# Kernel tuning notes

Hardware: AMD Instinct MI355X
Metric: run time of the kernel (lower is better)

Reference implementation:

```python
import jax, jax.numpy as jnp
import numpy as np

D_MODEL = 1024
D_K = 64
D_V = 64
N_HEADS = 16
LN_EPS = 1e-5


def setup_inputs() -> dict:
    key = jax.random.key(0)
    ks = jax.random.split(key, 9)
    B, S = 2, 2048
    scale = 0.02
    return {
        "input_Q": jax.random.normal(ks[0], (B, S, D_MODEL), dtype=jnp.float32),
        "input_K": jax.random.normal(ks[1], (B, S, D_MODEL), dtype=jnp.float32),
        "input_V": jax.random.normal(ks[2], (B, S, D_MODEL), dtype=jnp.float32),
        "W_Q": jax.random.normal(ks[3], (D_MODEL, N_HEADS * D_K), dtype=jnp.float32) * scale,
        "W_K": jax.random.normal(ks[4], (D_MODEL, N_HEADS * D_K), dtype=jnp.float32) * scale,
        "W_V": jax.random.normal(ks[5], (D_MODEL, N_HEADS * D_V), dtype=jnp.float32) * scale,
        "W_O": jax.random.normal(ks[6], (N_HEADS * D_V, D_MODEL), dtype=jnp.float32) * scale,
        "ln_gamma": jnp.ones((D_MODEL,), dtype=jnp.float32),
        "ln_beta": jnp.zeros((D_MODEL,), dtype=jnp.float32),
    }


def reference(input_Q, input_K, input_V, W_Q, W_K, W_V, W_O, ln_gamma, ln_beta):
    B, Lq, _ = input_Q.shape
    Lk = input_K.shape[1]
    # projections -> [B, H, L, d]
    Q = (input_Q @ W_Q).reshape(B, Lq, N_HEADS, D_K).transpose(0, 2, 1, 3)
    K = (input_K @ W_K).reshape(B, Lk, N_HEADS, D_K).transpose(0, 2, 1, 3)
    V = (input_V @ W_V).reshape(B, Lk, N_HEADS, D_V).transpose(0, 2, 1, 3)
    # scores: [B, H, Lq, Lk]
    scores = jnp.einsum("bhqd,bhkd->bhqk", Q, K) / jnp.sqrt(jnp.float32(D_K))
    # NOTE: source uses nn.Softmax(dim=1) -> softmax over the HEADS axis (faithful quirk)
    attn = jax.nn.softmax(scores, axis=1)
    context = jnp.einsum("bhqk,bhkv->bhqv", attn, V)
    context = context.transpose(0, 2, 1, 3).reshape(B, Lq, N_HEADS * D_V)
    output = context @ W_O
    # residual + LayerNorm over last dim
    x = output + input_Q
    mu = jnp.mean(x, axis=-1, keepdims=True)
    var = jnp.mean(jnp.square(x - mu), axis=-1, keepdims=True)
    return (x - mu) / jnp.sqrt(var + LN_EPS) * ln_gamma + ln_beta
```

## Files before the change

### kernel.cpp

```cpp
#include <hip/hip_runtime.h>
#include <cstdint>
#include <cstddef>

#define DM 1024
#define HEADS 16
#define DHEAD 64
#define SEQ 2048
#define BATCH 2

typedef __bf16 bf16x8 __attribute__((ext_vector_type(8)));
typedef float  f32x4  __attribute__((ext_vector_type(4)));
typedef unsigned short u16;
typedef unsigned int u32;
typedef u16 u16x8 __attribute__((ext_vector_type(8)));
typedef u16 u16x4 __attribute__((ext_vector_type(4)));

__device__ __forceinline__ float bf2f(u16 u){
    union { u32 i; float f; } v; v.i = ((u32)u) << 16; return v.f;
}
__device__ __forceinline__ u16 f2bf(float f){
    union { float f; u32 i; } v; v.f = f;
    u32 r = v.i + 0x7FFF + ((v.i >> 16) & 1);
    return (u16)(r >> 16);
}
__device__ __forceinline__ u16 f2bf_rhu(float f){
    union { float f; u32 i; } v; v.f = f;
    return (u16)((v.i + 0x8000u) >> 16);
}
__device__ __forceinline__ void gload16(const u16* g, u16* l){
    __builtin_amdgcn_global_load_lds(
        (const __attribute__((address_space(1))) u32*)g,
        (__attribute__((address_space(3))) u32*)l, 16, 0, 0);
}

__global__ void k_probe(const u16* __restrict__ q, int* __restrict__ hdr){
    if (threadIdx.x == 0 && blockIdx.x == 0){
        int cnt = 0;
        for (int i = 0; i < 256; i += 2){
            int e = (q[i] >> 7) & 0xFF;
            if (e >= 90 && e <= 141) cnt++;
        }
        hdr[0] = (cnt >= 64) ? 1 : 0;
        #pragma unroll
        for (int c = 1; c <= 8; c++) hdr[c] = 0;
    }
}

__global__ __launch_bounds__(256) void k_cvt3(const void* __restrict__ s0,
                                              const void* __restrict__ s1,
                                              const void* __restrict__ s2,
                                              u16* __restrict__ dstbase,
                                              const int* __restrict__ flag, int n){
    int z = blockIdx.y;
    const void* src = (z == 0) ? s0 : ((z == 1) ? s1 : s2);
    u16* dst = dstbase + (size_t)z * n;
    int i = (blockIdx.x * 256 + threadIdx.x) * 8;
    if (i >= n) return;
    if (*flag){
        *(u16x8*)&dst[i] = *(const u16x8*)((const u16*)src + i);
    } else {
        const float* s = (const float*)src + i;
        u16x8 o;
        #pragma unroll
        for (int j = 0; j < 8; j++) o[j] = f2bf(s[j]);
        *(u16x8*)&dst[i] = o;
    }
}

__global__ void k_tcvt4(const void* __restrict__ w0, const void* __restrict__ w1,
                        const void* __restrict__ w2, const void* __restrict__ w3,
                        u16* __restrict__ dstbase,
                        const int* __restrict__ flag, int R, int C){
    __shared__ u16 tile[32][33];
    int z = blockIdx.z;
    const void* src = (z == 0) ? w0 : ((z == 1) ? w1 : ((z == 2) ? w2 : w3));
    u16* dst = dstbase + (size_t)z * R * C;
    bool isbf = (*flag != 0);
    int c0 = blockIdx.x * 32, r0 = blockIdx.y * 32;
    int tx = threadIdx.x, ty = threadIdx.y;
    #pragma unroll
    for (int i = 0; i < 32; i += 8){
        size_t idx = (size_t)(r0 + ty + i) * C + c0 + tx;
        tile[ty + i][tx] = isbf ? ((const u16*)src)[idx] : f2bf(((const float*)src)[idx]);
    }
    __syncthreads();
    #pragma unroll
    for (int i = 0; i < 32; i += 8)
        dst[(size_t)(c0 + ty + i) * R + r0 + tx] = tile[tx][ty + i];
}

__global__ void k_transpose(const u16* __restrict__ src, u16* __restrict__ dst,
                            int R, int C){
    __shared__ u16 tile[32][33];
    size_t boff = (size_t)blockIdx.z * R * C;
    src += boff; dst += boff;
    int c0 = blockIdx.x * 32, r0 = blockIdx.y * 32;
    int tx = threadIdx.x, ty = threadIdx.y;
    #pragma unroll
    for (int i = 0; i < 32; i += 8)
        tile[ty + i][tx] = src[(size_t)(r0 + ty + i) * C + c0 + tx];
    __syncthreads();
    #pragma unroll
    for (int i = 0; i < 32; i += 8)
        dst[(size_t)(c0 + ty + i) * R + r0 + tx] = tile[tx][ty + i];
}

__global__ __launch_bounds__(256, 2) void k_gemm3z(const u16* __restrict__ A0,
                                                   const u16* __restrict__ Bt0,
                                                   u16* __restrict__ C0,
                                                   size_t strA, size_t strB, size_t strC,
                                                   int M, int N, int K){
    __shared__ u16 lsA[128 * 32];
    __shared__ u16 lsB[128 * 32];
    int z = blockIdx.z;
    const u16* A  = A0  + strA * z;
    const u16* Bt = Bt0 + strB * z;
    u16* C = C0 + strC * z;
    int m0 = blockIdx.y * 128, n0 = blockIdx.x * 128;
    int t = threadIdx.x, lane = t & 63, w = t >> 6;
    int l15 = lane & 15, quad = lane >> 4;
    int wm = (w & 1) * 64, wn = (w >> 1) * 64;
    int r0 = 32 * w + (lane >> 2);
    int r1 = r0 + 16;
    int c0s = (lane & 3) ^ (r0 & 3);
    int c1s = (lane & 3) ^ (r1 & 3);
    u16* dA0 = &lsA[(32 * w) * 32];
    u16* dA1 = &lsA[(32 * w + 16) * 32];
    u16* dB0 = &lsB[(32 * w) * 32];
    u16* dB1 = &lsB[(32 * w + 16) * 32];
    f32x4 acc[4][4] = {};
    for (int k0 = 0; k0 < K; k0 += 32){
        __syncthreads();
        gload16(&A [(size_t)(m0 + r0) * K + k0 + c0s * 8], dA0);
        gload16(&A [(size_t)(m0 + r1) * K + k0 + c1s * 8], dA1);
        gload16(&Bt[(size_t)(n0 + r0) * K + k0 + c0s * 8], dB0);
        gload16(&Bt[(size_t)(n0 + r1) * K + k0 + c1s * 8], dB1);
        __syncthreads();
        bf16x8 af[4], bfr[4];
        #pragma unroll
        for (int i = 0; i < 4; i++){
            int row = wm + i * 16 + l15;
            af[i] = *(const bf16x8*)&lsA[row * 32 + ((quad ^ (row & 3)) * 8)];
        }
        #pragma unroll
        for (int j = 0; j < 4; j++){
            int row = wn + j * 16 + l15;
            bfr[j] = *(const bf16x8*)&lsB[row * 32 + ((quad ^ (row & 3)) * 8)];
        }
        #pragma unroll
        for (int i = 0; i < 4; i++)
            #pragma unroll
            for (int j = 0; j < 4; j++)
                acc[i][j] = __builtin_amdgcn_mfma_f32_16x16x32_bf16(af[i], bfr[j], acc[i][j], 0, 0, 0);
    }
    #pragma unroll
    for (int i = 0; i < 4; i++)
        #pragma unroll
        for (int j = 0; j < 4; j++)
            #pragma unroll
            for (int r = 0; r < 4; r++){
                int m = m0 + wm + i * 16 + quad * 4 + r;
                int n = n0 + wn + j * 16 + l15;
                C[(size_t)m * N + n] = f2bf(acc[i][j][r]);
            }
}

__global__ __launch_bounds__(1024, 4) void k_attn5(const u16* __restrict__ Qp,
                                                   const u16* __restrict__ Kp,
                                                   const u16* __restrict__ Vt,
                                                   u16* __restrict__ c0,
                                                   u16* __restrict__ c1,
                                                   u16* __restrict__ c2,
                                                   u16* __restrict__ c3,
                                                   int* __restrict__ cnt,
                                                   int ncomboM1, int iters){
    __shared__ u16 ebuf[2][16][64][36];
    __shared__ int s_combo, s_slot;
    int t = threadIdx.x;
    if (t == 0){
        int xcc;
        asm volatile("s_getreg_b32 %0, hwreg(HW_REG_XCC_ID)" : "=s"(xcc));
        int start = xcc & ncomboM1;
        int combo = -1, slot = -1;
        for (int a = 0; a <= ncomboM1 && combo < 0; a++){
            int c = (start + a) & ncomboM1;
            int s = atomicAdd(&cnt[c], 1);
            if (s < 32){ combo = c; slot = s; }
        }
        s_combo = combo; s_slot = slot;
    }
    __syncthreads();
    int combo = s_combo;
    if (combo < 0) return;
    int b = combo & 1, chunk = combo >> 1;
    int q0 = s_slot * 64;
    int h = t >> 6, lane = t & 63, l15 = lane & 15, quad = lane >> 4;
    u16* outp = (chunk == 0) ? c0 : ((chunk == 1) ? c1 : ((chunk == 2) ? c2 : c3));
    const float cexp = 0.125f * 1.44269504f;
    int kbeg = chunk * (iters << 5);

    bf16x8 qf[4][2];
    #pragma unroll
    for (int sub = 0; sub < 4; sub++)
        #pragma unroll
        for (int ch = 0; ch < 2; ch++)
            qf[sub][ch] = *(const bf16x8*)&Qp[((size_t)(b * SEQ + q0 + sub * 16 + l15)) * DM
                                             + h * DHEAD + ch * 32 + quad * 8];

    f32x4 oacc[4][4] = {};
    int sq = t >> 4, sku = (t & 15) * 2;

    auto score_phase = [&](int it){
        int k0 = kbeg + (it << 5), bf = it & 1;
        #pragma unroll
        for (int kt = 0; kt < 2; kt++){
            const u16* kb = Kp + ((size_t)(b * SEQ + k0 + kt * 16 + l15)) * DM + h * DHEAD + quad * 8;
            bf16x8 kf0 = *(const bf16x8*)(kb);
            bf16x8 kf1 = *(const bf16x8*)(kb + 32);
            #pragma unroll
            for (int sub = 0; sub < 4; sub++){
                f32x4 sc = {};
                sc = __builtin_amdgcn_mfma_f32_16x16x32_bf16(qf[sub][0], kf0, sc, 0, 0, 0);
                sc = __builtin_amdgcn_mfma_f32_16x16x32_bf16(qf[sub][1], kf1, sc, 0, 0, 0);
                #pragma unroll
                for (int r = 0; r < 4; r++)
                    ebuf[bf][h][sub * 16 + quad * 4 + r][kt * 16 + l15] =
                        f2bf_rhu(exp2f(sc[r] * cexp));
            }
        }
    };

    score_phase(0);
    for (int it = 0; it < iters; it++){
        int bf = it & 1;
        __syncthreads();
        {
            u32 ev[16];
            float s0 = 0.f, s1 = 0.f;
            #pragma unroll
            for (int hh = 0; hh < 16; hh++){
                u32 u = *(const u32*)&ebuf[bf][hh][sq][sku];
                ev[hh] = u;
                union { u32 i; float f; } lo, hi;
                lo.i = u << 16; hi.i = u & 0xFFFF0000u;
                s0 += lo.f; s1 += hi.f;
            }
            float r0 = __builtin_amdgcn_rcpf(s0);
            float r1 = __builtin_amdgcn_rcpf(s1);
            #pragma unroll
            for (int hh = 0; hh < 16; hh++){
                union { u32 i; float f; } lo, hi, p0, p1;
                lo.i = ev[hh] << 16; hi.i = ev[hh] & 0xFFFF0000u;
                p0.f = lo.f * r0; p1.f = hi.f * r1;
                *(u32*)&ebuf[bf][hh][sq][sku] =
                    ((p0.i + 0x8000u) >> 16) | ((p1.i + 0x8000u) & 0xFFFF0000u);
            }
        }
        __syncthreads();
        int k0 = kbeg + (it << 5);
        bf16x8 pa[4];
        #pragma unroll
        for (int sub = 0; sub < 4; sub++){
            const u16* pp = &ebuf[bf][h][sub * 16 + l15][quad * 8];
            union { bf16x8 v; u16x4 q[2]; } pu;
            pu.q[0] = *(const u16x4*)pp;
            pu.q[1] = *(const u16x4*)(pp + 4);
            pa[sub] = pu.v;
        }
        #pragma unroll
        for (int vt = 0; vt < 4; vt++){
            bf16x8 vf = *(const bf16x8*)&Vt[((size_t)b * DM + h * DHEAD + vt * 16 + l15) * SEQ
                                            + k0 + quad * 8];
            #pragma unroll
            for (int sub = 0; sub < 4; sub++)
                oacc[sub][vt] = __builtin_amdgcn_mfma_f32_16x16x32_bf16(pa[sub], vf, oacc[sub][vt], 0, 0, 0);
        }
        if (it + 1 < iters) score_phase(it + 1);
    }
    #pragma unroll
    for (int sub = 0; sub < 4; sub++)
        #pragma unroll
        for (int vt = 0; vt < 4; vt++)
            #pragma unroll
            for (int r = 0; r < 4; r++){
                int q = q0 + sub * 16 + quad * 4 + r;
                int n = h * DHEAD + vt * 16 + l15;
                outp[((size_t)b * SEQ + q) * DM + n] = f2bf(oacc[sub][vt][r]);
            }
}

__global__ __launch_bounds__(256) void k_reduce(const u16* __restrict__ a,
                                                const u16* __restrict__ b,
                                                const u16* __restrict__ c,
                                                const u16* __restrict__ d,
                                                u16* __restrict__ dst, int n, int nch){
    int i = (blockIdx.x * 256 + threadIdx.x) * 8;
    if (i >= n) return;
    u16x8 x = *(const u16x8*)&a[i];
    u16x8 y = *(const u16x8*)&b[i];
    u16x8 o;
    if (nch == 4){
        u16x8 zc = *(const u16x8*)&c[i];
        u16x8 zd = *(const u16x8*)&d[i];
        #pragma unroll
        for (int j = 0; j < 8; j++)
            o[j] = f2bf((bf2f(x[j]) + bf2f(y[j])) + (bf2f(zc[j]) + bf2f(zd[j])));
    } else {
        #pragma unroll
        for (int j = 0; j < 8; j++) o[j] = f2bf(bf2f(x[j]) + bf2f(y[j]));
    }
    *(u16x8*)&dst[i] = o;
}

__global__ __launch_bounds__(256) void k_ln(const u16* __restrict__ O,
                                            const void* __restrict__ Qin,
                                            const void* __restrict__ gamma,
                                            const void* __restrict__ beta,
                                            void* __restrict__ out,
                                            const int* __restrict__ flag){
    __shared__ float red[4][2];
    bool isbf = (*flag != 0);
    int row = blockIdx.x;
    int t = threadIdx.x;
    const u16* op = O + (size_t)row * DM;
    float xv[4];
    float s1 = 0.f, s2 = 0.f;
    #pragma unroll
    for (int i = 0; i < 4; i++){
        int idx = i * 256 + t;
        float q = isbf ? bf2f(((const u16*)Qin)[(size_t)row * DM + idx])
                       : ((const float*)Qin)[(size_t)row * DM + idx];
        float x = bf2f(op[idx]) + q;
        xv[i] = x; s1 += x; s2 += x * x;
    }
    #pragma unroll
    for (int off = 32; off; off >>= 1){
        s1 += __shfl_down(s1, off);
        s2 += __shfl_down(s2, off);
    }
    int w = t >> 6, lane = t & 63;
    if (lane == 0){ red[w][0] = s1; red[w][1] = s2; }
    __syncthreads();
    float S1 = red[0][0] + red[1][0] + red[2][0] + red[3][0];
    float S2 = red[0][1] + red[1][1] + red[2][1] + red[3][1];
    float mu  = S1 * (1.0f / DM);
    float var = S2 * (1.0f / DM) - mu * mu;
    float rstd = rsqrtf(var + 1e-5f);
    #pragma unroll
    for (int i = 0; i < 4; i++){
        int idx = i * 256 + t;
        float g = isbf ? bf2f(((const u16*)gamma)[idx]) : ((const float*)gamma)[idx];
        float bb= isbf ? bf2f(((const u16*)beta )[idx]) : ((const float*)beta )[idx];
        float y = (xv[i] - mu) * rstd * g + bb;
        if (isbf) ((u16*)out)[(size_t)row * DM + idx] = f2bf(y);
        else      ((float*)out)[(size_t)row * DM + idx] = y;
    }
}

extern "C" void kernel_launch(void* const* d_in, const int* in_sizes, int n_in,
                              void* d_out, int out_size, void* d_ws, size_t ws_size,
                              hipStream_t stream){
    (void)in_sizes; (void)n_in; (void)out_size;
    const void* inQ = d_in[0];
    const void* inK = d_in[1];
    const void* inV = d_in[2];
    const void* wQ  = d_in[3];
    const void* wK  = d_in[4];
    const void* wV  = d_in[5];
    const void* wO  = d_in[6];
    const void* gma = d_in[7];
    const void* bta = d_in[8];

    int* hdr  = (int*)d_ws;
    int* flag = hdr;
    int* cnt  = hdr + 1;
    u16* base = (u16*)d_ws + 64;

    const size_t MB1 = 1024u * 1024u;
    const size_t M4  = 4u * MB1;
    u16* Qi  = base + 0;
    u16* Ki  = base + 1 * M4;
    u16* Vi  = base + 2 * M4;
    u16* WtQ = base + 3 * M4;
    u16* WtO = WtQ + 3 * MB1;
    u16* Qp  = base + 4 * M4;
    u16* Kp  = base + 5 * M4;
    u16* Vp  = base + 6 * M4;
    u16* ext = base + 7 * M4;
    u16* Vt    = Ki;
    u16* ctxp0 = Qi;
    u16* ctxp1 = Vp;
    u16* ctxp2 = Vi;

    size_t need4 = 128 + 8 * M4 * sizeof(u16);
    int nch = (ws_size >= need4) ? 4 : 2;
    u16* ctxp3 = (nch == 4) ? ext : ctxp2;
    int ncomboM1 = 2 * nch - 1;
    int iters   = (nch == 4) ? 16 : 32;
    int ablocks = 32 * 2 * nch;

    k_probe<<<1, 64, 0, stream>>>((const u16*)inQ, hdr);

    const int nIn = BATCH * SEQ * DM;
    k_cvt3<<<dim3(nIn / 2048, 3), 256, 0, stream>>>(inQ, inK, inV, base, flag, nIn);

    k_tcvt4<<<dim3(32, 32, 4), dim3(32, 8), 0, stream>>>(wQ, wK, wV, wO, WtQ, flag, 1024, 1024);

    k_gemm3z<<<dim3(8, 32, 3), 256, 0, stream>>>(Qi, WtQ, Qp, M4, MB1, M4, 4096, 1024, 1024);

    k_transpose<<<dim3(32, 64, 2), dim3(32, 8), 0, stream>>>(Vp, Vt, 2048, 1024);

    k_attn5<<<ablocks, 1024, 0, stream>>>(Qp, Kp, Vt, ctxp0, ctxp1, ctxp2, ctxp3,
                                          cnt, ncomboM1, iters);

    k_reduce<<<nIn / 2048, 256, 0, stream>>>(ctxp0, ctxp1, ctxp2, ctxp3, ctxp0, nIn, nch);

    k_gemm3z<<<dim3(8, 32, 1), 256, 0, stream>>>(ctxp0, WtO, Qp, 0, 0, 0, 4096, 1024, 1024);

    k_ln<<<4096, 256, 0, stream>>>(Qp, inQ, gma, bta, d_out, flag);
}
```

Before: 338.1 us.

## Halve attention block size to 32 queries with 8 waves covering two heads each

The heads-axis softmax attention kernel now uses 512-thread blocks that each handle 32 query rows, with each wave covering two heads. The grid doubles, so there are more, smaller blocks and less shared memory per block. The score MFMA operands are swapped so each lane holds four consecutive keys, letting the exp results be packed into one 8-byte LDS store instead of four scalar stores. The aim is better occupancy and load balance and fewer LDS write instructions, at the cost of reloading K/V tiles across twice as many blocks.

```diff
diff --git a/kernel.cpp b/kernel.cpp
--- a/kernel.cpp
+++ b/kernel.cpp
@@ -14,6 +14,7 @@
 typedef unsigned int u32;
 typedef u16 u16x8 __attribute__((ext_vector_type(8)));
 typedef u16 u16x4 __attribute__((ext_vector_type(4)));
+typedef u32 u32x2 __attribute__((ext_vector_type(2)));
 
 __device__ __forceinline__ float bf2f(u16 u){
     union { u32 i; float f; } v; v.i = ((u32)u) << 16; return v.f;
@@ -23,9 +24,9 @@
     u32 r = v.i + 0x7FFF + ((v.i >> 16) & 1);
     return (u16)(r >> 16);
 }
-__device__ __forceinline__ u16 f2bf_rhu(float f){
-    union { float f; u32 i; } v; v.f = f;
-    return (u16)((v.i + 0x8000u) >> 16);
+__device__ __forceinline__ u32 packbf2(float a, float b){
+    union { float f; u32 i; } x, y; x.f = a; y.f = b;
+    return ((x.i + 0x8000u) >> 16) | ((y.i + 0x8000u) & 0xFFFF0000u);
 }
 __device__ __forceinline__ void gload16(const u16* g, u16* l){
     __builtin_amdgcn_global_load_lds(
@@ -165,16 +166,16 @@
             }
 }
 
-__global__ __launch_bounds__(1024, 4) void k_attn5(const u16* __restrict__ Qp,
-                                                   const u16* __restrict__ Kp,
-                                                   const u16* __restrict__ Vt,
-                                                   u16* __restrict__ c0,
-                                                   u16* __restrict__ c1,
-                                                   u16* __restrict__ c2,
-                                                   u16* __restrict__ c3,
-                                                   int* __restrict__ cnt,
-                                                   int ncomboM1, int iters){
-    __shared__ u16 ebuf[2][16][64][36];
+__global__ __launch_bounds__(512, 4) void k_attn6(const u16* __restrict__ Qp,
+                                                  const u16* __restrict__ Kp,
+                                                  const u16* __restrict__ Vt,
+                                                  u16* __restrict__ c0,
+                                                  u16* __restrict__ c1,
+                                                  u16* __restrict__ c2,
+                                                  u16* __restrict__ c3,
+                                                  int* __restrict__ cnt,
+                                                  int ncomboM1, int iters, int capM1){
+    __shared__ u16 ebuf[2][16][32][36];
     __shared__ int s_combo, s_slot;
     int t = threadIdx.x;
     if (t == 0){
@@ -185,7 +186,7 @@
         for (int a = 0; a <= ncomboM1 && combo < 0; a++){
             int c = (start + a) & ncomboM1;
             int s = atomicAdd(&cnt[c], 1);
-            if (s < 32){ combo = c; slot = s; }
+            if (s <= capM1){ combo = c; slot = s; }
         }
         s_combo = combo; s_slot = slot;
     }
@@ -193,39 +194,49 @@
     int combo = s_combo;
     if (combo < 0) return;
     int b = combo & 1, chunk = combo >> 1;
-    int q0 = s_slot * 64;
-    int h = t >> 6, lane = t & 63, l15 = lane & 15, quad = lane >> 4;
+    int q0 = s_slot * 32;
+    int w = t >> 6, lane = t & 63, l15 = lane & 15, quad = lane >> 4;
     u16* outp = (chunk == 0) ? c0 : ((chunk == 1) ? c1 : ((chunk == 2) ? c2 : c3));
     const float cexp = 0.125f * 1.44269504f;
     int kbeg = chunk * (iters << 5);
 
-    bf16x8 qf[4][2];
-    #pragma unroll
-    for (int sub = 0; sub < 4; sub++)
-        #pragma unroll
-        for (int ch = 0; ch < 2; ch++)
-            qf[sub][ch] = *(const bf16x8*)&Qp[((size_t)(b * SEQ + q0 + sub * 16 + l15)) * DM
-                                             + h * DHEAD + ch * 32 + quad * 8];
-
-    f32x4 oacc[4][4] = {};
+    bf16x8 qf[2][2][2];
+    #pragma unroll
+    for (int hd = 0; hd < 2; hd++){
+        int h = w + hd * 8;
+        #pragma unroll
+        for (int sub = 0; sub < 2; sub++)
+            #pragma unroll
+            for (int ch = 0; ch < 2; ch++)
+                qf[hd][sub][ch] = *(const bf16x8*)&Qp[((size_t)(b * SEQ + q0 + sub * 16 + l15)) * DM
+                                                     + h * DHEAD + ch * 32 + quad * 8];
+    }
+
+    f32x4 oacc[2][2][4] = {};
     int sq = t >> 4, sku = (t & 15) * 2;
 
     auto score_phase = [&](int it){
         int k0 = kbeg + (it << 5), bf = it & 1;
         #pragma unroll
-        for (int kt = 0; kt < 2; kt++){
-            const u16* kb = Kp + ((size_t)(b * SEQ + k0 + kt * 16 + l15)) * DM + h * DHEAD + quad * 8;
-            bf16x8 kf0 = *(const bf16x8*)(kb);
-            bf16x8 kf1 = *(const bf16x8*)(kb + 32);
-            #pragma unroll
-            for (int sub = 0; sub < 4; sub++){
-                f32x4 sc = {};
-                sc = __builtin_amdgcn_mfma_f32_16x16x32_bf16(qf[sub][0], kf0, sc, 0, 0, 0);
-                sc = __builtin_amdgcn_mfma_f32_16x16x32_bf16(qf[sub][1], kf1, sc, 0, 0, 0);
+        for (int hd = 0; hd < 2; hd++){
+            int h = w + hd * 8;
+            #pragma unroll
+            for (int kt = 0; kt < 2; kt++){
+                const u16* kb = Kp + ((size_t)(b * SEQ + k0 + kt * 16 + l15)) * DM + h * DHEAD + quad * 8;
+                bf16x8 kf0 = *(const bf16x8*)(kb);
+                bf16x8 kf1 = *(const bf16x8*)(kb + 32);
                 #pragma unroll
-                for (int r = 0; r < 4; r++)
-                    ebuf[bf][h][sub * 16 + quad * 4 + r][kt * 16 + l15] =
-                        f2bf_rhu(exp2f(sc[r] * cexp));
+                for (int sub = 0; sub < 2; sub++){
+                    f32x4 sc = {};
+                    sc = __builtin_amdgcn_mfma_f32_16x16x32_bf16(kf0, qf[hd][sub][0], sc, 0, 0, 0);
+                    sc = __builtin_amdgcn_mfma_f32_16x16x32_bf16(kf1, qf[hd][sub][1], sc, 0, 0, 0);
+                    float e0 = exp2f(sc[0] * cexp);
+                    float e1 = exp2f(sc[1] * cexp);
+                    float e2 = exp2f(sc[2] * cexp);
+                    float e3 = exp2f(sc[3] * cexp);
+                    u32x2 pk; pk[0] = packbf2(e0, e1); pk[1] = packbf2(e2, e3);
+                    *(u32x2*)&ebuf[bf][h][sub * 16 + l15][kt * 16 + quad * 4] = pk;
+                }
             }
         }
     };
@@ -258,35 +269,42 @@
         }
         __syncthreads();
         int k0 = kbeg + (it << 5);
-        bf16x8 pa[4];
-        #pragma unroll
-        for (int sub = 0; sub < 4; sub++){
-            const u16* pp = &ebuf[bf][h][sub * 16 + l15][quad * 8];
-            union { bf16x8 v; u16x4 q[2]; } pu;
-            pu.q[0] = *(const u16x4*)pp;
-            pu.q[1] = *(const u16x4*)(pp + 4);
-            pa[sub] = pu.v;
-        }
-        #pragma unroll
-        for (int vt = 0; vt < 4; vt++){
-            bf16x8 vf = *(const bf16x8*)&Vt[((size_t)b * DM + h * DHEAD + vt * 16 + l15) * SEQ
-                                            + k0 + quad * 8];
-            #pragma unroll
-            for (int sub = 0; sub < 4; sub++)
-                oacc[sub][vt] = __builtin_amdgcn_mfma_f32_16x16x32_bf16(pa[sub], vf, oacc[sub][vt], 0, 0, 0);
+        #pragma unroll
+        for (int hd = 0; hd < 2; hd++){
+            int h = w + hd * 8;
+            bf16x8 pa[2];
+            #pragma unroll
+            for (int sub = 0; sub < 2; sub++){
+                const u16* pp = &ebuf[bf][h][sub * 16 + l15][quad * 8];
+                union { bf16x8 v; u16x4 q[2]; } pu;
+                pu.q[0] = *(const u16x4*)pp;
+                pu.q[1] = *(const u16x4*)(pp + 4);
+                pa[sub] = pu.v;
+            }
+            #pragma unroll
+            for (int vt = 0; vt < 4; vt++){
+                bf16x8 vf = *(const bf16x8*)&Vt[((size_t)b * DM + h * DHEAD + vt * 16 + l15) * SEQ
+                                                + k0 + quad * 8];
+                oacc[hd][0][vt] = __builtin_amdgcn_mfma_f32_16x16x32_bf16(pa[0], vf, oacc[hd][0][vt], 0, 0, 0);
+                oacc[hd][1][vt] = __builtin_amdgcn_mfma_f32_16x16x32_bf16(pa[1], vf, oacc[hd][1][vt], 0, 0, 0);
+            }
         }
         if (it + 1 < iters) score_phase(it + 1);
     }
     #pragma unroll
-    for (int sub = 0; sub < 4; sub++)
-        #pragma unroll
-        for (int vt = 0; vt < 4; vt++)
-            #pragma unroll
-            for (int r = 0; r < 4; r++){
-                int q = q0 + sub * 16 + quad * 4 + r;
-                int n = h * DHEAD + vt * 16 + l15;
-                outp[((size_t)b * SEQ + q) * DM + n] = f2bf(oacc[sub][vt][r]);
-            }
+    for (int hd = 0; hd < 2; hd++){
+        int h = w + hd * 8;
+        #pragma unroll
+        for (int sub = 0; sub < 2; sub++)
+            #pragma unroll
+            for (int vt = 0; vt < 4; vt++)
+                #pragma unroll
+                for (int r = 0; r < 4; r++){
+                    int q = q0 + sub * 16 + quad * 4 + r;
+                    int n = h * DHEAD + vt * 16 + l15;
+                    outp[((size_t)b * SEQ + q) * DM + n] = f2bf(oacc[hd][sub][vt][r]);
+                }
+    }
 }
 
 __global__ __launch_bounds__(256) void k_reduce(const u16* __restrict__ a,
@@ -397,7 +415,8 @@
     u16* ctxp3 = (nch == 4) ? ext : ctxp2;
     int ncomboM1 = 2 * nch - 1;
     int iters   = (nch == 4) ? 16 : 32;
-    int ablocks = 32 * 2 * nch;
+    int ablocks = 64 * 2 * nch;
+    int capM1   = 63;
 
     k_probe<<<1, 64, 0, stream>>>((const u16*)inQ, hdr);
 
@@ -410,8 +429,8 @@
 
     k_transpose<<<dim3(32, 64, 2), dim3(32, 8), 0, stream>>>(Vp, Vt, 2048, 1024);
 
-    k_attn5<<<ablocks, 1024, 0, stream>>>(Qp, Kp, Vt, ctxp0, ctxp1, ctxp2, ctxp3,
-                                          cnt, ncomboM1, iters);
+    k_attn6<<<ablocks, 512, 0, stream>>>(Qp, Kp, Vt, ctxp0, ctxp1, ctxp2, ctxp3,
+                                         cnt, ncomboM1, iters, capM1);
 
     k_reduce<<<nIn / 2048, 256, 0, stream>>>(ctxp0, ctxp1, ctxp2, ctxp3, ctxp0, nIn, nch);
 
```

Measured after the change: 391.6 us. 15.8% more time.

## Merge prep kernels, fuse V transpose into projection GEMM, pack score stores

Applied to the files above, without the earlier changes.

Merges the input conversion and weight-transpose kernels into one launch, and makes the QKV projection GEMM write V directly in transposed layout so the separate transpose kernel is gone. The attention score phase swaps MFMA operand order so each lane holds consecutive key columns and stores packed bf16 pairs as 64-bit LDS writes instead of scalar 16-bit writes. This removes two launches plus a full read/write pass over V. In exchange, the transposed V stores from the GEMM are strided and less coalesced, and buffer aliasing is reassigned.

```diff
diff --git a/kernel.cpp b/kernel.cpp
--- a/kernel.cpp
+++ b/kernel.cpp
@@ -14,6 +14,7 @@
 typedef unsigned int u32;
 typedef u16 u16x8 __attribute__((ext_vector_type(8)));
 typedef u16 u16x4 __attribute__((ext_vector_type(4)));
+typedef u32 u32x2 __attribute__((ext_vector_type(2)));
 
 __device__ __forceinline__ float bf2f(u16 u){
     union { u32 i; float f; } v; v.i = ((u32)u) << 16; return v.f;
@@ -23,9 +24,9 @@
     u32 r = v.i + 0x7FFF + ((v.i >> 16) & 1);
     return (u16)(r >> 16);
 }
-__device__ __forceinline__ u16 f2bf_rhu(float f){
-    union { float f; u32 i; } v; v.f = f;
-    return (u16)((v.i + 0x8000u) >> 16);
+__device__ __forceinline__ u32 packbf2(float a, float b){
+    union { float f; u32 i; } x, y; x.f = a; y.f = b;
+    return ((x.i + 0x8000u) >> 16) | ((y.i + 0x8000u) & 0xFFFF0000u);
 }
 __device__ __forceinline__ void gload16(const u16* g, u16* l){
     __builtin_amdgcn_global_load_lds(
@@ -41,81 +42,69 @@
             if (e >= 90 && e <= 141) cnt++;
         }
         hdr[0] = (cnt >= 64) ? 1 : 0;
-        #pragma unroll
-        for (int c = 1; c <= 8; c++) hdr[c] = 0;
-    }
-}
-
-__global__ __launch_bounds__(256) void k_cvt3(const void* __restrict__ s0,
-                                              const void* __restrict__ s1,
-                                              const void* __restrict__ s2,
-                                              u16* __restrict__ dstbase,
-                                              const int* __restrict__ flag, int n){
-    int z = blockIdx.y;
-    const void* src = (z == 0) ? s0 : ((z == 1) ? s1 : s2);
-    u16* dst = dstbase + (size_t)z * n;
-    int i = (blockIdx.x * 256 + threadIdx.x) * 8;
-    if (i >= n) return;
-    if (*flag){
-        *(u16x8*)&dst[i] = *(const u16x8*)((const u16*)src + i);
+    }
+}
+
+__global__ __launch_bounds__(256) void k_prep(const void* __restrict__ iQ,
+                                              const void* __restrict__ iK,
+                                              const void* __restrict__ iV,
+                                              const void* __restrict__ w0,
+                                              const void* __restrict__ w1,
+                                              const void* __restrict__ w2,
+                                              const void* __restrict__ w3,
+                                              u16* __restrict__ base,
+                                              u16* __restrict__ wtbase,
+                                              int* __restrict__ hdr, int nIn){
+    __shared__ u16 tile[32][33];
+    int bid = blockIdx.x, t = threadIdx.x;
+    bool isbf = (hdr[0] != 0);
+    if (bid == 0 && t < 8) hdr[1 + t] = 0;
+    if (bid < 6144){
+        int z = bid >> 11;
+        const void* src = (z == 0) ? iQ : ((z == 1) ? iK : iV);
+        u16* dst = base + (size_t)z * nIn;
+        int i = ((bid & 2047) * 256 + t) * 8;
+        if (isbf){
+            *(u16x8*)&dst[i] = *(const u16x8*)((const u16*)src + i);
+        } else {
+            const float* s = (const float*)src + i;
+            u16x8 o;
+            #pragma unroll
+            for (int j = 0; j < 8; j++) o[j] = f2bf(s[j]);
+            *(u16x8*)&dst[i] = o;
+        }
     } else {
-        const float* s = (const float*)src + i;
-        u16x8 o;
-        #pragma unroll
-        for (int j = 0; j < 8; j++) o[j] = f2bf(s[j]);
-        *(u16x8*)&dst[i] = o;
-    }
-}
-
-__global__ void k_tcvt4(const void* __restrict__ w0, const void* __restrict__ w1,
-                        const void* __restrict__ w2, const void* __restrict__ w3,
-                        u16* __restrict__ dstbase,
-                        const int* __restrict__ flag, int R, int C){
-    __shared__ u16 tile[32][33];
-    int z = blockIdx.z;
-    const void* src = (z == 0) ? w0 : ((z == 1) ? w1 : ((z == 2) ? w2 : w3));
-    u16* dst = dstbase + (size_t)z * R * C;
-    bool isbf = (*flag != 0);
-    int c0 = blockIdx.x * 32, r0 = blockIdx.y * 32;
-    int tx = threadIdx.x, ty = threadIdx.y;
-    #pragma unroll
-    for (int i = 0; i < 32; i += 8){
-        size_t idx = (size_t)(r0 + ty + i) * C + c0 + tx;
-        tile[ty + i][tx] = isbf ? ((const u16*)src)[idx] : f2bf(((const float*)src)[idx]);
-    }
-    __syncthreads();
-    #pragma unroll
-    for (int i = 0; i < 32; i += 8)
-        dst[(size_t)(c0 + ty + i) * R + r0 + tx] = tile[tx][ty + i];
-}
-
-__global__ void k_transpose(const u16* __restrict__ src, u16* __restrict__ dst,
-                            int R, int C){
-    __shared__ u16 tile[32][33];
-    size_t boff = (size_t)blockIdx.z * R * C;
-    src += boff; dst += boff;
-    int c0 = blockIdx.x * 32, r0 = blockIdx.y * 32;
-    int tx = threadIdx.x, ty = threadIdx.y;
-    #pragma unroll
-    for (int i = 0; i < 32; i += 8)
-        tile[ty + i][tx] = src[(size_t)(r0 + ty + i) * C + c0 + tx];
-    __syncthreads();
-    #pragma unroll
-    for (int i = 0; i < 32; i += 8)
-        dst[(size_t)(c0 + ty + i) * R + r0 + tx] = tile[tx][ty + i];
+        int bid2 = bid - 6144;
+        int z = bid2 >> 10, tl = bid2 & 1023;
+        const void* src = (z == 0) ? w0 : ((z == 1) ? w1 : ((z == 2) ? w2 : w3));
+        u16* dst = wtbase + (size_t)z * DM * DM;
+        int c0 = (tl & 31) * 32, r0 = (tl >> 5) * 32;
+        int tx = t & 31, ty = t >> 5;
+        #pragma unroll
+        for (int i = 0; i < 32; i += 8){
+            size_t idx = (size_t)(r0 + ty + i) * DM + c0 + tx;
+            tile[ty + i][tx] = isbf ? ((const u16*)src)[idx] : f2bf(((const float*)src)[idx]);
+        }
+        __syncthreads();
+        #pragma unroll
+        for (int i = 0; i < 32; i += 8)
+            dst[(size_t)(c0 + ty + i) * DM + r0 + tx] = tile[tx][ty + i];
+    }
 }
 
 __global__ __launch_bounds__(256, 2) void k_gemm3z(const u16* __restrict__ A0,
                                                    const u16* __restrict__ Bt0,
-                                                   u16* __restrict__ C0,
-                                                   size_t strA, size_t strB, size_t strC,
-                                                   int M, int N, int K){
+                                                   u16* __restrict__ Cq,
+                                                   u16* __restrict__ Ck,
+                                                   u16* __restrict__ Cv,
+                                                   size_t strA, size_t strB,
+                                                   int K, int vtrans){
     __shared__ u16 lsA[128 * 32];
     __shared__ u16 lsB[128 * 32];
     int z = blockIdx.z;
     const u16* A  = A0  + strA * z;
     const u16* Bt = Bt0 + strB * z;
-    u16* C = C0 + strC * z;
+    u16* C = (z == 0) ? Cq : ((z == 1) ? Ck : Cv);
     int m0 = blockIdx.y * 128, n0 = blockIdx.x * 128;
     int t = threadIdx.x, lane = t & 63, w = t >> 6;
     int l15 = lane & 15, quad = lane >> 4;
@@ -153,19 +142,35 @@
             for (int j = 0; j < 4; j++)
                 acc[i][j] = __builtin_amdgcn_mfma_f32_16x16x32_bf16(af[i], bfr[j], acc[i][j], 0, 0, 0);
     }
-    #pragma unroll
-    for (int i = 0; i < 4; i++)
-        #pragma unroll
-        for (int j = 0; j < 4; j++)
-            #pragma unroll
-            for (int r = 0; r < 4; r++){
-                int m = m0 + wm + i * 16 + quad * 4 + r;
+    if (vtrans && z == 2){
+        #pragma unroll
+        for (int i = 0; i < 4; i++){
+            int m = m0 + wm + i * 16 + quad * 4;
+            int bb = m >> 11, s = m & 2047;
+            #pragma unroll
+            for (int j = 0; j < 4; j++){
                 int n = n0 + wn + j * 16 + l15;
-                C[(size_t)m * N + n] = f2bf(acc[i][j][r]);
+                u16x4 o;
+                #pragma unroll
+                for (int r = 0; r < 4; r++) o[r] = f2bf(acc[i][j][r]);
+                *(u16x4*)&C[((size_t)bb * DM + n) * SEQ + s] = o;
             }
-}
-
-__global__ __launch_bounds__(1024, 4) void k_attn5(const u16* __restrict__ Qp,
+        }
+    } else {
+        #pragma unroll
+        for (int i = 0; i < 4; i++)
+            #pragma unroll
+            for (int j = 0; j < 4; j++)
+                #pragma unroll
+                for (int r = 0; r < 4; r++){
+                    int m = m0 + wm + i * 16 + quad * 4 + r;
+                    int n = n0 + wn + j * 16 + l15;
+                    C[(size_t)m * DM + n] = f2bf(acc[i][j][r]);
+                }
+    }
+}
+
+__global__ __launch_bounds__(1024, 4) void k_attn7(const u16* __restrict__ Qp,
                                                    const u16* __restrict__ Kp,
                                                    const u16* __restrict__ Vt,
                                                    u16* __restrict__ c0,
@@ -220,12 +225,12 @@
             #pragma unroll
             for (int sub = 0; sub < 4; sub++){
                 f32x4 sc = {};
-                sc = __builtin_amdgcn_mfma_f32_16x16x32_bf16(qf[sub][0], kf0, sc, 0, 0, 0);
-                sc = __builtin_amdgcn_mfma_f32_16x16x32_bf16(qf[sub][1], kf1, sc, 0, 0, 0);
-                #pragma unroll
-                for (int r = 0; r < 4; r++)
-                    ebuf[bf][h][sub * 16 + quad * 4 + r][kt * 16 + l15] =
-                        f2bf_rhu(exp2f(sc[r] * cexp));
+                sc = __builtin_amdgcn_mfma_f32_16x16x32_bf16(kf0, qf[sub][0], sc, 0, 0, 0);
+                sc = __builtin_amdgcn_mfma_f32_16x16x32_bf16(kf1, qf[sub][1], sc, 0, 0, 0);
+                u32x2 pk;
+                pk[0] = packbf2(exp2f(sc[0] * cexp), exp2f(sc[1] * cexp));
+                pk[1] = packbf2(exp2f(sc[2] * cexp), exp2f(sc[3] * cexp));
+                *(u32x2*)&ebuf[bf][h][sub * 16 + l15][kt * 16 + quad * 4] = pk;
             }
         }
     };
@@ -385,11 +390,10 @@
     u16* WtO = WtQ + 3 * MB1;
     u16* Qp  = base + 4 * M4;
     u16* Kp  = base + 5 * M4;
-    u16* Vp  = base + 6 * M4;
+    u16* Vt  = base + 6 * M4;
     u16* ext = base + 7 * M4;
-    u16* Vt    = Ki;
     u16* ctxp0 = Qi;
-    u16* ctxp1 = Vp;
+    u16* ctxp1 = Ki;
     u16* ctxp2 = Vi;
 
     size_t need4 = 128 + 8 * M4 * sizeof(u16);
@@ -402,20 +406,19 @@
     k_probe<<<1, 64, 0, stream>>>((const u16*)inQ, hdr);
 
     const int nIn = BATCH * SEQ * DM;
-    k_cvt3<<<dim3(nIn / 2048, 3), 256, 0, stream>>>(inQ, inK, inV, base, flag, nIn);
-
-    k_tcvt4<<<dim3(32, 32, 4), dim3(32, 8), 0, stream>>>(wQ, wK, wV, wO, WtQ, flag, 1024, 1024);
-
-    k_gemm3z<<<dim3(8, 32, 3), 256, 0, stream>>>(Qi, WtQ, Qp, M4, MB1, M4, 4096, 1024, 1024);
-
-    k_transpose<<<dim3(32, 64, 2), dim3(32, 8), 0, stream>>>(Vp, Vt, 2048, 1024);
-
-    k_attn5<<<ablocks, 1024, 0, stream>>>(Qp, Kp, Vt, ctxp0, ctxp1, ctxp2, ctxp3,
+    k_prep<<<10240, 256, 0, stream>>>(inQ, inK, inV, wQ, wK, wV, wO,
+                                      base, WtQ, hdr, nIn);
+
+    k_gemm3z<<<dim3(8, 32, 3), 256, 0, stream>>>(Qi, WtQ, Qp, Kp, Vt,
+                                                 M4, MB1, 1024, 1);
+
+    k_attn7<<<ablocks, 1024, 0, stream>>>(Qp, Kp, Vt, ctxp0, ctxp1, ctxp2, ctxp3,
                                           cnt, ncomboM1, iters);
 
     k_reduce<<<nIn / 2048, 256, 0, stream>>>(ctxp0, ctxp1, ctxp2, ctxp3, ctxp0, nIn, nch);
 
-    k_gemm3z<<<dim3(8, 32, 1), 256, 0, stream>>>(ctxp0, WtO, Qp, 0, 0, 0, 4096, 1024, 1024);
+    k_gemm3z<<<dim3(8, 32, 1), 256, 0, stream>>>(ctxp0, WtO, Qp, Qp, Qp,
+                                                 0, 0, 1024, 0);
 
     k_ln<<<4096, 256, 0, stream>>>(Qp, inQ, gma, bta, d_out, flag);
 }
```

Measured after the change: 347.3 us. 2.7% more time.
